# Optimization experiments

Hardware: AMD Instinct MI355X
Metric: run time of the kernel (lower is better)

The kernel has to match this reference:

```python
import jax, jax.numpy as jnp
import numpy as np

N, C, H, W = 32, 256, 64, 64
STRIDE = 4  # slices of refs' H dim per block, as in the torch mem_save path
EPS = 1e-12  # F.normalize clamp_min eps


def setup_inputs() -> dict:
    key = jax.random.key(0)
    k1, k2 = jax.random.split(key)
    refs = jax.random.normal(k1, (N, C, H, W), dtype=jnp.float32)
    img = jax.random.normal(k2, (C, H, W), dtype=jnp.float32)
    return {"refs": refs, "img": img}


def _l2_normalize(x, axis):
    # matches torch.nn.functional.normalize(p=2): x / max(||x||, eps)
    n = jnp.sqrt(jnp.sum(x * x, axis=axis, keepdims=True))
    return x / jnp.maximum(n, EPS)


def reference(refs, img):
    # refs: (N, C, H, W), img: (C, H, W)
    refs_n = _l2_normalize(refs, axis=1)
    img_n = _l2_normalize(img, axis=0)

    img_flat = img_n.reshape(C, H * W).T  # (HW, C) query vectors

    # group reference feature vectors by blocks of STRIDE rows of refs' H dim:
    # (N,C,H,W) -> (H, N, W, C) -> (H//STRIDE, STRIDE*N*W, C)
    blocks = refs_n.transpose(2, 0, 3, 1).reshape(H // STRIDE, STRIDE * N * W, C)

    def step(running_max, block):
        # (HW, C) x (blocksize, C)^T -> (HW, blocksize) cosine sims
        sim = jnp.einsum('xc,yc->xy', img_flat, block)
        return jnp.maximum(running_max, sim.max(axis=1)), None

    init = jnp.full((H * W,), -jnp.inf, dtype=img_flat.dtype)
    best, _ = jax.lax.scan(step, init, blocks)
    return best.reshape(H, W)
```

## Files before the change

kernel.cpp:

```cpp
#include <hip/hip_runtime.h>

#define CN 256
#define HN 64
#define WN 64
#define NNW 32
#define HW (HN*WN)
#define NREF (NNW*HW)
#define KD 256

#define BM2 128
#define BN2 128
#define NCH 16
#define NTILES (NREF/NCH/BN2)

using bf16x8 = __attribute__((ext_vector_type(8))) short;
using f32x4  = __attribute__((ext_vector_type(4))) float;

__device__ inline unsigned short f2bf(float x) {
  unsigned int u = __float_as_uint(x);
  return (unsigned short)((u + 0x7fffu + ((u >> 16) & 1u)) >> 16);
}

__device__ inline void atomicMaxFloat(float* addr, float val) {
  if (val >= 0.f) atomicMax(reinterpret_cast<int*>(addr), __float_as_int(val));
  else            atomicMin(reinterpret_cast<unsigned int*>(addr), __float_as_uint(val));
}

__device__ inline void gload_lds16(const void* g, void* l) {
  __builtin_amdgcn_global_load_lds(
      (const __attribute__((address_space(1))) void*)g,
      (__attribute__((address_space(3))) void*)l, 16, 0, 0);
}

__global__ __launch_bounds__(256)
void norm_kernel(const float* __restrict__ refs, const float* __restrict__ img,
                 unsigned short* __restrict__ Rb, unsigned short* __restrict__ Qb,
                 float* __restrict__ out) {
  __shared__ float tile[CN][WN + 1];
  __shared__ float ssq[4][WN];
  __shared__ float scl[WN];
  const int bid = blockIdx.x;
  const int t = threadIdx.x;
  const float* src; unsigned short* dst; int nh;
  if (bid < NNW * HN) { src = refs; dst = Rb; nh = bid; }
  else {
    src = img; dst = Qb; nh = bid - NNW * HN;
    if (t < 64) out[(size_t)nh * 64 + t] = -INFINITY;
  }
  const float* base = src + (size_t)(nh >> 6) * (CN * (size_t)HW) + (size_t)(nh & 63) * WN;

  const int c16 = t >> 4, w4 = (t & 15) * 4;
#pragma unroll
  for (int j = 0; j < 16; ++j) {
    int c = j * 16 + c16;
    float4 v = *(const float4*)&base[(size_t)c * HW + w4];
    tile[c][w4 + 0] = v.x; tile[c][w4 + 1] = v.y;
    tile[c][w4 + 2] = v.z; tile[c][w4 + 3] = v.w;
  }
  __syncthreads();
  {
    int w = t & 63, vv = t >> 6;
    float s = 0.f;
#pragma unroll 8
    for (int cc = 0; cc < 64; ++cc) { float x = tile[vv * 64 + cc][w]; s += x * x; }
    ssq[vv][w] = s;
  }
  __syncthreads();
  if (t < 64)
    scl[t] = 1.f / fmaxf(sqrtf(ssq[0][t] + ssq[1][t] + ssq[2][t] + ssq[3][t]), 1e-12f);
  __syncthreads();
  const int w = t >> 2, cq = t & 3;
  unsigned short* orow = dst + ((size_t)nh * WN + w) * KD;
  const float sc = scl[w];
#pragma unroll
  for (int j = 0; j < 8; ++j) {
    int c0 = (j * 4 + cq) * 8;
    bf16x8 o;
#pragma unroll
    for (int k = 0; k < 8; ++k) o[k] = (short)f2bf(tile[c0 + k][w] * sc);
    *(bf16x8*)&orow[c0] = o;
  }
}

#define BARR() __builtin_amdgcn_s_barrier()
#define SCHED0() __builtin_amdgcn_sched_barrier(0)
#define GATE(N) asm volatile("s_waitcnt vmcnt(" #N ")" ::: "memory")
#define LGKM0() asm volatile("s_waitcnt lgkmcnt(0)" ::: "memory")

#define STG4(SUB, PTR, KOFF) do { \
  _Pragma("unroll") \
  for (int p = 0; p < 4; ++p) \
    gload_lds16((PTR) + (KOFF) + p * 8 * KD, &lds[SUB][(w * 32 + p * 8) * 64]); \
} while (0)

#define HALF(SUB, J, ACM0) do { \
  bf16x8 bb[2][4]; \
  _Pragma("unroll") \
  for (int ks = 0; ks < 2; ++ks) \
  _Pragma("unroll") \
  for (int ni = 0; ni < 4; ++ni) \
    bb[ks][ni] = *(const bf16x8*)&lds[SUB][(nrow + ni * 16) * 64 + (ks ? (pk0 ^ 32) : pk0)]; \
  __builtin_amdgcn_s_setprio(1); \
  _Pragma("unroll") \
  for (int ks = 0; ks < 2; ++ks) \
  _Pragma("unroll") \
  for (int mi = 0; mi < 4; ++mi) \
  _Pragma("unroll") \
  for (int ni = 0; ni < 4; ++ni) \
    acc[mi][ni] = __builtin_amdgcn_mfma_f32_16x16x32_bf16(a[mi][(SUB)*2 + ks], bb[ks][ni], \
                      ((ACM0) || (J) || ks) ? acc[mi][ni] : ZZ, 0, 0, 0); \
  __builtin_amdgcn_s_setprio(0); \
} while (0)

#define PH(PAIR, ACM0, STGM, GN) do { \
  if ((STGM) == 1) { STG4(2, rs, 128); STG4(3, rs, 192); } \
  if ((STGM) == 2) { STG4(0, rs + 32768, 0); STG4(1, rs + 32768, 64); } \
  GATE(GN); BARR(); SCHED0(); \
  HALF((PAIR)*2,     0, ACM0); \
  HALF((PAIR)*2 + 1, 1, ACM0); \
  SCHED0(); BARR(); \
} while (0)

#define FOLD() do { \
  _Pragma("unroll") \
  for (int mi = 0; mi < 4; ++mi) \
  _Pragma("unroll") \
  for (int ee = 0; ee < 4; ++ee) { \
    float v0 = fmaxf(acc[mi][0][ee], acc[mi][1][ee]); \
    float v1 = fmaxf(acc[mi][2][ee], acc[mi][3][ee]); \
    run[mi][ee] = fmaxf(run[mi][ee], fmaxf(v0, v1)); \
  } \
} while (0)

__global__ __launch_bounds__(256, 2)
void simmax_kernel(const unsigned short* __restrict__ Q,
                   const unsigned short* __restrict__ R,
                   float* __restrict__ out) {
  __shared__ unsigned short lds[4][8192];

  const int t = threadIdx.x;
  const int lane = t & 63;
  const int w  = t >> 6;
  const int wm = w >> 1;
  const int wn = w & 1;

  const int wg  = (blockIdx.x & 7) * 64 + (blockIdx.x >> 3);
  const int nch = wg >> 5;
  const int bm  = wg & 31;

  const int srow = lane >> 3;
  const int schunk = (lane & 7) ^ srow;
  const unsigned short* qsrcA = Q + (size_t)(bm * BM2 + w * 32 + srow) * KD + schunk * 8;
  const unsigned short* rsrc0 = R + (size_t)((size_t)nch * (NTILES * BN2) + w * 32 + srow) * KD + schunk * 8;

  const int pk0 = (((lane >> 4) ^ (lane & 7))) * 8;
  const int mrow = wm * 64 + (lane & 15);
  const int nrow = wn * 64 + (lane & 15);

  const f32x4 ZZ = {0.f, 0.f, 0.f, 0.f};
  f32x4 acc[4][4];
  f32x4 run[4];
#pragma unroll
  for (int mi = 0; mi < 4; ++mi)
#pragma unroll
    for (int ee = 0; ee < 4; ++ee) run[mi][ee] = -1e30f;

#pragma unroll
  for (int s = 0; s < 4; ++s)
    STG4(s, qsrcA, s * 64);
  GATE(0); BARR(); SCHED0();

  bf16x8 a[4][8];
#pragma unroll
  for (int mi = 0; mi < 4; ++mi) {
    const int rb = (mrow + mi * 16) * 64;
#pragma unroll
    for (int kq = 0; kq < 4; ++kq) {
      a[mi][kq * 2 + 0] = *(const bf16x8*)&lds[kq][rb + pk0];
      a[mi][kq * 2 + 1] = *(const bf16x8*)&lds[kq][rb + (pk0 ^ 32)];
    }
  }
  LGKM0(); BARR();

  const unsigned short* rs = rsrc0;
  STG4(0, rs, 0); STG4(1, rs, 64);

  for (int bt = 0; bt < NTILES - 1; ++bt) {
    PH(0, 0, 1, 8);
    PH(1, 1, 2, 8);
    FOLD();
    rs += 32768;
  }
  PH(0, 0, 1, 8);
  PH(1, 1, 0, 0);
  FOLD();

#pragma unroll
  for (int mi = 0; mi < 4; ++mi)
#pragma unroll
  for (int ee = 0; ee < 4; ++ee) {
    float v = run[mi][ee];
    v = fmaxf(v, __shfl_xor(v, 1));
    v = fmaxf(v, __shfl_xor(v, 2));
    v = fmaxf(v, __shfl_xor(v, 4));
    v = fmaxf(v, __shfl_xor(v, 8));
    if ((lane & 15) == 0)
      atomicMaxFloat(&out[bm * BM2 + wm * 64 + mi * 16 + (lane >> 4) * 4 + ee], v);
  }
}

extern "C" void kernel_launch(void* const* d_in, const int* in_sizes, int n_in,
                              void* d_out, int out_size, void* d_ws, size_t ws_size,
                              hipStream_t stream) {
  const float* refs = (const float*)d_in[0];
  const float* img  = (const float*)d_in[1];
  float* out = (float*)d_out;

  unsigned short* Rb = (unsigned short*)d_ws;
  unsigned short* Qb = Rb + (size_t)NREF * KD;

  hipLaunchKernelGGL(norm_kernel, dim3(NNW * HN + HN), dim3(256), 0, stream,
                     refs, img, Rb, Qb, out);
  hipLaunchKernelGGL(simmax_kernel, dim3(NCH * (HW / BM2)), dim3(256), 0, stream,
                     Qb, Rb, out);
}
```

Baseline: 254.2 us.

## Enlarge query tile to 256 rows with 8-wave blocks and double-buffered ref tiles

```diff
diff --git a/kernel.cpp b/kernel.cpp
--- a/kernel.cpp
+++ b/kernel.cpp
@@ -8,10 +8,10 @@
 #define NREF (NNW*HW)
 #define KD 256
 
-#define BM2 128
-#define BN2 128
-#define NCH 16
-#define NTILES (NREF/NCH/BN2)
+#define BMT 256
+#define BNT 128
+#define NCHV 16
+#define NTILES (NREF/NCHV/BNT)
 
 using bf16x8 = __attribute__((ext_vector_type(8))) short;
 using f32x4  = __attribute__((ext_vector_type(4))) float;
@@ -87,78 +87,65 @@
 #define GATE(N) asm volatile("s_waitcnt vmcnt(" #N ")" ::: "memory")
 #define LGKM0() asm volatile("s_waitcnt lgkmcnt(0)" ::: "memory")
 
-#define STG4(SUB, PTR, KOFF) do { \
-  _Pragma("unroll") \
-  for (int p = 0; p < 4; ++p) \
-    gload_lds16((PTR) + (KOFF) + p * 8 * KD, &lds[SUB][(w * 32 + p * 8) * 64]); \
+#define STGB(P, TOFF) do { \
+  _Pragma("unroll") \
+  for (int q = 0; q < 8; ++q) \
+    gload_lds16(rsb + (TOFF) + q * 8 * KD, \
+                &lds[(P) * 4 + (wid >> 1)][(wid & 1) * 4096 + q * 512]); \
 } while (0)
 
-#define HALF(SUB, J, ACM0) do { \
-  bf16x8 bb[2][4]; \
-  _Pragma("unroll") \
-  for (int ks = 0; ks < 2; ++ks) \
-  _Pragma("unroll") \
-  for (int ni = 0; ni < 4; ++ni) \
-    bb[ks][ni] = *(const bf16x8*)&lds[SUB][(nrow + ni * 16) * 64 + (ks ? (pk0 ^ 32) : pk0)]; \
+#define STRIP(P, NI) do { \
+  bf16x8 bb[8]; \
+  _Pragma("unroll") \
+  for (int kf = 0; kf < 8; ++kf) \
+    bb[kf] = *(const bf16x8*)&lds[(P) * 4 + (kf >> 1)] \
+        [(nrow + (NI) * 16) * 64 + (((kf & 1) * 4 + (lane >> 4)) ^ l7) * 8]; \
+  f32x4 acc[4]; \
   __builtin_amdgcn_s_setprio(1); \
   _Pragma("unroll") \
-  for (int ks = 0; ks < 2; ++ks) \
+  for (int kf = 0; kf < 8; ++kf) \
   _Pragma("unroll") \
   for (int mi = 0; mi < 4; ++mi) \
-  _Pragma("unroll") \
-  for (int ni = 0; ni < 4; ++ni) \
-    acc[mi][ni] = __builtin_amdgcn_mfma_f32_16x16x32_bf16(a[mi][(SUB)*2 + ks], bb[ks][ni], \
-                      ((ACM0) || (J) || ks) ? acc[mi][ni] : ZZ, 0, 0, 0); \
+    acc[mi] = __builtin_amdgcn_mfma_f32_16x16x32_bf16(a[mi][kf], bb[kf], \
+                  kf ? acc[mi] : ZZ, 0, 0, 0); \
   __builtin_amdgcn_s_setprio(0); \
+  _Pragma("unroll") \
+  for (int mi = 0; mi < 4; ++mi) \
+  _Pragma("unroll") \
+  for (int ee = 0; ee < 4; ++ee) \
+    run[mi][ee] = fmaxf(run[mi][ee], acc[mi][ee]); \
 } while (0)
 
-#define PH(PAIR, ACM0, STGM, GN) do { \
-  if ((STGM) == 1) { STG4(2, rs, 128); STG4(3, rs, 192); } \
-  if ((STGM) == 2) { STG4(0, rs + 32768, 0); STG4(1, rs + 32768, 64); } \
-  GATE(GN); BARR(); SCHED0(); \
-  HALF((PAIR)*2,     0, ACM0); \
-  HALF((PAIR)*2 + 1, 1, ACM0); \
-  SCHED0(); BARR(); \
-} while (0)
-
-#define FOLD() do { \
-  _Pragma("unroll") \
-  for (int mi = 0; mi < 4; ++mi) \
-  _Pragma("unroll") \
-  for (int ee = 0; ee < 4; ++ee) { \
-    float v0 = fmaxf(acc[mi][0][ee], acc[mi][1][ee]); \
-    float v1 = fmaxf(acc[mi][2][ee], acc[mi][3][ee]); \
-    run[mi][ee] = fmaxf(run[mi][ee], fmaxf(v0, v1)); \
-  } \
-} while (0)
-
-__global__ __launch_bounds__(256, 2)
+#define STRIPS(P) do { STRIP(P, 0); STRIP(P, 1); STRIP(P, 2); STRIP(P, 3); } while (0)
+
+__global__ __launch_bounds__(512, 2)
 void simmax_kernel(const unsigned short* __restrict__ Q,
                    const unsigned short* __restrict__ R,
                    float* __restrict__ out) {
-  __shared__ unsigned short lds[4][8192];
+  __shared__ unsigned short lds[8][8192];
 
   const int t = threadIdx.x;
   const int lane = t & 63;
-  const int w  = t >> 6;
-  const int wm = w >> 1;
-  const int wn = w & 1;
-
-  const int wg  = (blockIdx.x & 7) * 64 + (blockIdx.x >> 3);
-  const int nch = wg >> 5;
-  const int bm  = wg & 31;
+  const int wid = t >> 6;
+  const int wm = wid >> 1;
+  const int wn = wid & 1;
+  const int l7 = lane & 7;
+
+  const int wg  = (blockIdx.x & 7) * 32 + (blockIdx.x >> 3);
+  const int nch = wg >> 4;
+  const int bm  = wg & 15;
 
   const int srow = lane >> 3;
   const int schunk = (lane & 7) ^ srow;
-  const unsigned short* qsrcA = Q + (size_t)(bm * BM2 + w * 32 + srow) * KD + schunk * 8;
-  const unsigned short* rsrc0 = R + (size_t)((size_t)nch * (NTILES * BN2) + w * 32 + srow) * KD + schunk * 8;
-
-  const int pk0 = (((lane >> 4) ^ (lane & 7))) * 8;
+  const unsigned short* qsb = Q + (size_t)(bm * BMT + (wid >> 2) * 128 + srow) * KD
+                                + (wid & 3) * 64 + schunk * 8;
+  const unsigned short* rsb = R + (size_t)((size_t)nch * (NTILES * BNT) + (wid & 1) * 64 + srow) * KD
+                                + (wid >> 1) * 64 + schunk * 8;
+
   const int mrow = wm * 64 + (lane & 15);
   const int nrow = wn * 64 + (lane & 15);
 
   const f32x4 ZZ = {0.f, 0.f, 0.f, 0.f};
-  f32x4 acc[4][4];
   f32x4 run[4];
 #pragma unroll
   for (int mi = 0; mi < 4; ++mi)
@@ -166,34 +153,31 @@
     for (int ee = 0; ee < 4; ++ee) run[mi][ee] = -1e30f;
 
 #pragma unroll
-  for (int s = 0; s < 4; ++s)
-    STG4(s, qsrcA, s * 64);
+  for (int p = 0; p < 16; ++p)
+    gload_lds16(qsb + p * 8 * KD, &lds[wid][p * 512]);
   GATE(0); BARR(); SCHED0();
 
   bf16x8 a[4][8];
 #pragma unroll
   for (int mi = 0; mi < 4; ++mi) {
-    const int rb = (mrow + mi * 16) * 64;
-#pragma unroll
-    for (int kq = 0; kq < 4; ++kq) {
-      a[mi][kq * 2 + 0] = *(const bf16x8*)&lds[kq][rb + pk0];
-      a[mi][kq * 2 + 1] = *(const bf16x8*)&lds[kq][rb + (pk0 ^ 32)];
-    }
+    const int sub4 = ((wm * 4 + mi) >> 3) * 4;
+    const int r7 = (mrow + mi * 16) & 127;
+#pragma unroll
+    for (int kf = 0; kf < 8; ++kf)
+      a[mi][kf] = *(const bf16x8*)&lds[sub4 + (kf >> 1)]
+          [r7 * 64 + (((kf & 1) * 4 + (lane >> 4)) ^ l7) * 8];
   }
   LGKM0(); BARR();
 
-  const unsigned short* rs = rsrc0;
-  STG4(0, rs, 0); STG4(1, rs, 64);
-
+  STGB(0, 0);
   for (int bt = 0; bt < NTILES - 1; ++bt) {
-    PH(0, 0, 1, 8);
-    PH(1, 1, 2, 8);
-    FOLD();
-    rs += 32768;
-  }
-  PH(0, 0, 1, 8);
-  PH(1, 1, 0, 0);
-  FOLD();
+    STGB((bt + 1) & 1, (bt + 1) * (BNT * KD));
+    GATE(8); BARR(); SCHED0();
+    STRIPS(bt & 1);
+    BARR();
+  }
+  GATE(0); BARR(); SCHED0();
+  STRIPS((NTILES - 1) & 1);
 
 #pragma unroll
   for (int mi = 0; mi < 4; ++mi)
@@ -205,7 +189,7 @@
     v = fmaxf(v, __shfl_xor(v, 4));
     v = fmaxf(v, __shfl_xor(v, 8));
     if ((lane & 15) == 0)
-      atomicMaxFloat(&out[bm * BM2 + wm * 64 + mi * 16 + (lane >> 4) * 4 + ee], v);
+      atomicMaxFloat(&out[bm * BMT + wm * 64 + mi * 16 + (lane >> 4) * 4 + ee], v);
   }
 }
 
@@ -221,6 +205,6 @@
 
   hipLaunchKernelGGL(norm_kernel, dim3(NNW * HN + HN), dim3(256), 0, stream,
                      refs, img, Rb, Qb, out);
-  hipLaunchKernelGGL(simmax_kernel, dim3(NCH * (HW / BM2)), dim3(256), 0, stream,
+  hipLaunchKernelGGL(simmax_kernel, dim3(NCHV * (HW / BMT)), dim3(512), 0, stream,
                      Qb, Rb, out);
 }
```

Result: faster. 222.6 us (-12.4%).
